# Optimization experiments

Measured on AMD Instinct MI355X. Metric: run time of the kernel, lower is better.

Reference implementation:

```python
import jax, jax.numpy as jnp
import numpy as np

D_MODEL = 2048
NUM_HEADS = 16
D_K = D_MODEL // NUM_HEADS
MAX_SEQ_LEN = 2048


def setup_inputs() -> dict:
    key = jax.random.key(0)
    ks = jax.random.split(key, 9)
    s = 1.0 / np.sqrt(D_MODEL)
    x = jax.random.normal(ks[0], (4, 2048, D_MODEL), dtype=jnp.float32)
    Wq = jax.random.normal(ks[1], (D_MODEL, D_MODEL), dtype=jnp.float32) * s
    bq = jnp.zeros((D_MODEL,), dtype=jnp.float32)
    Wk = jax.random.normal(ks[2], (D_MODEL, D_MODEL), dtype=jnp.float32) * s
    bk = jnp.zeros((D_MODEL,), dtype=jnp.float32)
    Wv = jax.random.normal(ks[3], (D_MODEL, D_MODEL), dtype=jnp.float32) * s
    bv = jnp.zeros((D_MODEL,), dtype=jnp.float32)
    Wo = jax.random.normal(ks[4], (D_MODEL, D_MODEL), dtype=jnp.float32) * s
    bo = jnp.zeros((D_MODEL,), dtype=jnp.float32)
    return {"x": x, "Wq": Wq, "bq": bq, "Wk": Wk, "bk": bk,
            "Wv": Wv, "bv": bv, "Wo": Wo, "bo": bo}


def _rope_tables(seq_len, d_k, dtype):
    # GPT-NeoX style rotate-half RoPE tables: [seq_len, d_k]
    inv_freq = 1.0 / (10000.0 ** (np.arange(0, d_k, 2, dtype=np.float32) / d_k))
    pos = np.arange(seq_len, dtype=np.float32)
    freqs = np.outer(pos, inv_freq)              # [S, d_k/2]
    emb = np.concatenate([freqs, freqs], axis=-1)  # [S, d_k]
    return jnp.asarray(np.cos(emb), dtype=dtype), jnp.asarray(np.sin(emb), dtype=dtype)


def _apply_rope(x, cos, sin):
    # x: [B, H, S, d_k]; rotate-half
    x1, x2 = jnp.split(x, 2, axis=-1)
    rotated = jnp.concatenate([-x2, x1], axis=-1)
    return x * cos + rotated * sin


def reference(x, Wq, bq, Wk, bk, Wv, bv, Wo, bo):
    B, S, _ = x.shape
    cos, sin = _rope_tables(S, D_K, x.dtype)  # [S, d_k]

    def split_heads(t):  # [B,S,D] -> [B,H,S,d_k]
        return t.reshape(B, S, NUM_HEADS, D_K).transpose(0, 2, 1, 3)

    q = split_heads(x @ Wq.T + bq)
    k = split_heads(x @ Wk.T + bk)
    v = split_heads(x @ Wv.T + bv)

    q = _apply_rope(q, cos, sin)
    k = _apply_rope(k, cos, sin)

    scale = 1.0 / jnp.sqrt(jnp.asarray(D_K, dtype=x.dtype))
    scores = jnp.einsum("bhqd,bhkd->bhqk", q, k) * scale
    attn = jax.nn.softmax(scores, axis=-1)
    out = jnp.einsum("bhqk,bhkd->bhqd", attn, v)  # [B,H,S,d_k]
    out = out.transpose(0, 2, 1, 3).reshape(B, S, D_MODEL)
    return out @ Wo.T + bo
```

## Files before the change

### kernel.cpp

```cpp
#include <hip/hip_runtime.h>
#include <hip/hip_bf16.h>
#include <math.h>

typedef __bf16 bf16;
typedef __bf16 bf16x2 __attribute__((ext_vector_type(2)));
typedef __bf16 bf16x4 __attribute__((ext_vector_type(4)));
typedef __bf16 bf16x8 __attribute__((ext_vector_type(8)));
typedef float f32x4 __attribute__((ext_vector_type(4)));

#define D_MODEL 2048
#define SEQ 2048
#define BATCH 4
#define NH 16
#define DK 128

typedef const __attribute__((address_space(1))) void* as1_ptr;
typedef __attribute__((address_space(3))) void* as3_ptr;

__device__ __forceinline__ void gld_lds16(const bf16* g, bf16* l) {
  __builtin_amdgcn_global_load_lds((as1_ptr)g, (as3_ptr)l, 16, 0, 0);
}

__global__ void cvt_kernel(const float* __restrict__ in, bf16* __restrict__ out, int n8) {
  int i = blockIdx.x * 256 + threadIdx.x;
  if (i >= n8) return;
  long base = (long)i * 8;
  const float4* p = (const float4*)(in + base);
  float4 a = p[0], b = p[1];
  bf16x8 v;
  v[0] = (bf16)a.x; v[1] = (bf16)a.y; v[2] = (bf16)a.z; v[3] = (bf16)a.w;
  v[4] = (bf16)b.x; v[5] = (bf16)b.y; v[6] = (bf16)b.z; v[7] = (bf16)b.w;
  *(bf16x8*)(out + base) = v;
}

__global__ void cvt4_kernel(const float* a, const float* b, const float* c, const float* d,
                            bf16* oa, bf16* ob, bf16* oc, bf16* od) {
  const float* in; bf16* out;
  switch (blockIdx.y) {
    case 0: in = a; out = oa; break;
    case 1: in = b; out = ob; break;
    case 2: in = c; out = oc; break;
    default: in = d; out = od; break;
  }
  int i = blockIdx.x * 256 + threadIdx.x;
  long base = (long)i * 8;
  const float4* p = (const float4*)(in + base);
  float4 x = p[0], y = p[1];
  bf16x8 v;
  v[0] = (bf16)x.x; v[1] = (bf16)x.y; v[2] = (bf16)x.z; v[3] = (bf16)x.w;
  v[4] = (bf16)y.x; v[5] = (bf16)y.y; v[6] = (bf16)y.z; v[7] = (bf16)y.w;
  *(bf16x8*)(out + base) = v;
}

template<int OUT_F32, int BIAS_ROW>
__global__ __launch_bounds__(256, 2)
void gemm_nt(const bf16* __restrict__ A, const bf16* __restrict__ B,
             const float* __restrict__ bias, void* __restrict__ Cout, int K, int ldc)
{
  __shared__ alignas(16) bf16 As[128 * 32];
  __shared__ alignas(16) bf16 Bs[128 * 32];
  const int tid  = threadIdx.x;
  const int wave = tid >> 6, lane = tid & 63;
  const int quad = lane >> 4, l16 = lane & 15;
  const int n0 = blockIdx.x * 128, m0 = blockIdx.y * 128;
  const int wm = (wave >> 1) * 64, wn = (wave & 1) * 64;

  const int srow = tid >> 2, scol = (tid & 3) * 8;
  const bf16* Ag1 = A + (long)(m0 + srow) * K + scol;
  const bf16* Ag2 = Ag1 + (long)64 * K;
  const bf16* Bg1 = B + (long)(n0 + srow) * K + scol;
  const bf16* Bg2 = Bg1 + (long)64 * K;
  bf16* Asw = As + wave * 512;
  bf16* Bsw = Bs + wave * 512;

  f32x4 acc[4][4] = {};
  for (int k0 = 0; k0 < K; k0 += 32) {
    __syncthreads();
    gld_lds16(Ag1 + k0, Asw);
    gld_lds16(Ag2 + k0, Asw + 2048);
    gld_lds16(Bg1 + k0, Bsw);
    gld_lds16(Bg2 + k0, Bsw + 2048);
    __syncthreads();
    bf16x8 Af[4], Bf[4];
    for (int mi = 0; mi < 4; mi++)
      Af[mi] = *(const bf16x8*)(&As[(wm + mi * 16 + l16) * 32 + quad * 8]);
    for (int ni = 0; ni < 4; ni++)
      Bf[ni] = *(const bf16x8*)(&Bs[(wn + ni * 16 + l16) * 32 + quad * 8]);
    for (int mi = 0; mi < 4; mi++)
      for (int ni = 0; ni < 4; ni++)
        acc[mi][ni] = __builtin_amdgcn_mfma_f32_16x16x32_bf16(Af[mi], Bf[ni], acc[mi][ni], 0, 0, 0);
  }

  float bv[4];
  if (!BIAS_ROW)
    for (int ni = 0; ni < 4; ni++) bv[ni] = bias[n0 + wn + ni * 16 + l16];
  for (int mi = 0; mi < 4; mi++)
    for (int r = 0; r < 4; r++) {
      long row = m0 + wm + mi * 16 + quad * 4 + r;
      float bm = BIAS_ROW ? bias[row] : 0.0f;
      for (int ni = 0; ni < 4; ni++) {
        float v = acc[mi][ni][r] + (BIAS_ROW ? bm : bv[ni]);
        long idx = row * (long)ldc + n0 + wn + ni * 16 + l16;
        if (OUT_F32) ((float*)Cout)[idx] = v;
        else         ((bf16*)Cout)[idx] = (bf16)v;
      }
    }
}

__global__ void ropetab_kernel(float* __restrict__ ctab) {
  int idx = blockIdx.x * 256 + threadIdx.x;
  int j = idx & 63, p = idx >> 6;
  float f = exp2f(-(float)j * 0.20762050593046f);
  float th = (float)p * f;
  ctab[idx * 2]     = cosf(th);
  ctab[idx * 2 + 1] = sinf(th);
}

__global__ void rope_kernel(bf16* __restrict__ Q, bf16* __restrict__ K,
                            const float* __restrict__ ctab) {
  long idx = (long)blockIdx.x * 256 + threadIdx.x;
  bf16* P = blockIdx.y ? K : Q;
  int i2 = (int)(idx & 31);
  int h  = (int)((idx >> 5) & 15);
  long row = idx >> 9;
  int pos = (int)(row & (SEQ - 1));
  float4 cs = *(const float4*)(ctab + ((long)pos * 64 + 2 * i2) * 2);
  long base = row * D_MODEL + h * DK + 2 * i2;
  bf16x2 x1 = *(bf16x2*)(P + base);
  bf16x2 x2 = *(bf16x2*)(P + base + 64);
  bf16x2 y1, y2;
  y1[0] = (bf16)((float)x1[0] * cs.x - (float)x2[0] * cs.y);
  y2[0] = (bf16)((float)x2[0] * cs.x + (float)x1[0] * cs.y);
  y1[1] = (bf16)((float)x1[1] * cs.z - (float)x2[1] * cs.w);
  y2[1] = (bf16)((float)x2[1] * cs.z + (float)x1[1] * cs.w);
  *(bf16x2*)(P + base)      = y1;
  *(bf16x2*)(P + base + 64) = y2;
}

__global__ __launch_bounds__(256, 2)
void attn_kernel(const bf16* __restrict__ Q, const bf16* __restrict__ K,
                 const bf16* __restrict__ Vt, bf16* __restrict__ O)
{
  __shared__ alignas(16) bf16 Ks[2][64 * 128];
  __shared__ alignas(16) bf16 Vts[2][128 * 64];
  __shared__ alignas(16) bf16 Ps[128 * 36];
  const int tid  = threadIdx.x;
  const int wave = tid >> 6, lane = tid & 63;
  const int quad = lane >> 4, l16 = lane & 15;
  const int qt = blockIdx.x, bh = blockIdx.y;
  const int b = bh >> 4, h = bh & 15;
  const long qrow0 = (long)b * SEQ + qt * 128;
  const bf16* Qb = Q + qrow0 * D_MODEL + h * DK;
  const bf16* Kb = K + (long)b * SEQ * D_MODEL + h * DK;
  const bf16* Vb = Vt + (long)(h * DK) * (BATCH * SEQ) + b * SEQ;

  bf16x8 Qf[2][4];
  for (int ni = 0; ni < 2; ni++)
    for (int ks = 0; ks < 4; ks++)
      Qf[ni][ks] = *(const bf16x8*)(Qb + (long)(wave * 32 + ni * 16 + l16) * D_MODEL + ks * 32 + quad * 8);

  const bf16* Ksrc[4]; const bf16* Vsrc[4];
  for (int i = 0; i < 4; i++) {
    int g = wave * 4 + i;
    int rk = 4 * g + (lane >> 4);
    int ck = l16 ^ (rk & 7);
    Ksrc[i] = Kb + (long)rk * D_MODEL + ck * 8;
    int rv = 8 * g + (lane >> 3);
    int cv = (lane & 7) ^ (rv & 7);
    Vsrc[i] = Vb + (long)rv * (BATCH * SEQ) + cv * 8;
  }

  f32x4 Oacc[8][2] = {};
  float lsum[2] = {0.0f, 0.0f};
  const float kSc = 0.088388347648318447f * 1.4426950408889634f;
  const int swz = l16 & 7;

  for (int i = 0; i < 4; i++) gld_lds16(Ksrc[i], &Ks[0][(wave * 4 + i) * 512]);
  for (int i = 0; i < 4; i++) gld_lds16(Vsrc[i], &Vts[0][(wave * 4 + i) * 512]);
  __syncthreads();

  int cur = 0;
  for (int kt = 64; kt <= SEQ; kt += 64) {
    if (kt < SEQ) {
      for (int i = 0; i < 4; i++)
        gld_lds16(Ksrc[i] + (long)kt * D_MODEL, &Ks[cur ^ 1][(wave * 4 + i) * 512]);
      for (int i = 0; i < 4; i++)
        gld_lds16(Vsrc[i] + kt, &Vts[cur ^ 1][(wave * 4 + i) * 512]);
    }
    const bf16* Ksb = Ks[cur];
    const bf16* Vsb = Vts[cur];

    for (int hh = 0; hh < 2; hh++) {
      f32x4 Sc[2][2] = {};
      __builtin_amdgcn_s_setprio(1);
      for (int ks = 0; ks < 4; ks++) {
        bf16x8 Kf[2];
        for (int j = 0; j < 2; j++) {
          int si = hh * 2 + j;
          int c = (ks * 4 + quad) ^ swz;
          Kf[j] = *(const bf16x8*)(&Ksb[(si * 16 + l16) * 128 + c * 8]);
        }
        for (int j = 0; j < 2; j++)
          for (int ni = 0; ni < 2; ni++)
            Sc[j][ni] = __builtin_amdgcn_mfma_f32_16x16x32_bf16(Kf[j], Qf[ni][ks], Sc[j][ni], 0, 0, 0);
      }
      __builtin_amdgcn_s_setprio(0);

      for (int j = 0; j < 2; j++)
        for (int ni = 0; ni < 2; ni++) {
          bf16x4 pk;
          for (int r = 0; r < 4; r++) {
            float p = exp2f(Sc[j][ni][r] * kSc);
            lsum[ni] += p;
            pk[r] = (bf16)p;
          }
          *(bf16x4*)(&Ps[(wave * 32 + ni * 16 + l16) * 36 + j * 16 + quad * 4]) = pk;
        }

      __builtin_amdgcn_s_setprio(1);
      bf16x8 Pf[2];
      for (int ni = 0; ni < 2; ni++)
        Pf[ni] = *(const bf16x8*)(&Ps[(wave * 32 + ni * 16 + l16) * 36 + quad * 8]);
      for (int mi = 0; mi < 8; mi++) {
        int c = (hh * 4 + quad) ^ swz;
        bf16x8 Vf = *(const bf16x8*)(&Vsb[(mi * 16 + l16) * 64 + c * 8]);
        for (int ni = 0; ni < 2; ni++)
          Oacc[mi][ni] = __builtin_amdgcn_mfma_f32_16x16x32_bf16(Vf, Pf[ni], Oacc[mi][ni], 0, 0, 0);
      }
      __builtin_amdgcn_s_setprio(0);
    }

    __syncthreads();
    cur ^= 1;
  }

  for (int ni = 0; ni < 2; ni++) {
    lsum[ni] += __shfl_xor(lsum[ni], 16);
    lsum[ni] += __shfl_xor(lsum[ni], 32);
  }

  for (int ni = 0; ni < 2; ni++) {
    float rinv = 1.0f / lsum[ni];
    long rowbase = (qrow0 + wave * 32 + ni * 16 + l16) * (long)D_MODEL + h * DK + quad * 4;
    for (int mi = 0; mi < 8; mi++) {
      bf16x4 o;
      for (int r = 0; r < 4; r++) o[r] = (bf16)(Oacc[mi][ni][r] * rinv);
      *(bf16x4*)(O + rowbase + mi * 16) = o;
    }
  }
}

extern "C" void kernel_launch(void* const* d_in, const int* in_sizes, int n_in,
                              void* d_out, int out_size, void* d_ws, size_t ws_size,
                              hipStream_t stream) {
  const float* x  = (const float*)d_in[0];
  const float* Wq = (const float*)d_in[1];
  const float* bq = (const float*)d_in[2];
  const float* Wk = (const float*)d_in[3];
  const float* bk = (const float*)d_in[4];
  const float* Wv = (const float*)d_in[5];
  const float* bv = (const float*)d_in[6];
  const float* Wo = (const float*)d_in[7];
  const float* bo = (const float*)d_in[8];
  float* out = (float*)d_out;

  bf16* ws = (bf16*)d_ws;
  bf16* xb  = ws;
  bf16* Wqb = ws + 16777216;
  bf16* Wkb = ws + 20971520;
  bf16* Wvb = ws + 25165824;
  bf16* Wob = ws + 29360128;
  bf16* Qp  = ws + 33554432;
  bf16* Kp  = ws + 50331648;
  bf16* VtF = ws + 67108864;
  float* ctab = (float*)ws;
  bf16* O   = xb;

  cvt_kernel<<<8192, 256, 0, stream>>>(x, xb, 2097152);
  cvt4_kernel<<<dim3(2048, 4), 256, 0, stream>>>(Wq, Wk, Wv, Wo, Wqb, Wkb, Wvb, Wob);

  dim3 gg(16, 64);
  gemm_nt<0, 0><<<gg, 256, 0, stream>>>(xb, Wqb, bq, Qp, 2048, 2048);
  gemm_nt<0, 0><<<gg, 256, 0, stream>>>(xb, Wkb, bk, Kp, 2048, 2048);
  gemm_nt<0, 1><<<dim3(64, 16), 256, 0, stream>>>(Wvb, xb, bv, VtF, 2048, 8192);

  ropetab_kernel<<<512, 256, 0, stream>>>(ctab);
  rope_kernel<<<dim3(16384, 2), 256, 0, stream>>>(Qp, Kp, ctab);

  attn_kernel<<<dim3(16, 64), 256, 0, stream>>>(Qp, Kp, VtF, O);

  gemm_nt<1, 0><<<gg, 256, 0, stream>>>(O, Wob, bo, out, 2048, 2048);
}
```

Baseline: 697.4 us.

## Replace GEMM with 256x256 tiled, double-buffered, swizzled LDS kernel

```diff
diff --git a/kernel.cpp b/kernel.cpp
--- a/kernel.cpp
+++ b/kernel.cpp
@@ -53,48 +53,93 @@
 }
 
 template<int OUT_F32, int BIAS_ROW>
-__global__ __launch_bounds__(256, 2)
-void gemm_nt(const bf16* __restrict__ A, const bf16* __restrict__ B,
+__global__ __launch_bounds__(512, 2)
+void gemm256(const bf16* __restrict__ A, const bf16* __restrict__ B,
              const float* __restrict__ bias, void* __restrict__ Cout, int K, int ldc)
 {
-  __shared__ alignas(16) bf16 As[128 * 32];
-  __shared__ alignas(16) bf16 Bs[128 * 32];
+  __shared__ alignas(16) bf16 As[2][256 * 64];
+  __shared__ alignas(16) bf16 Bs[2][256 * 64];
   const int tid  = threadIdx.x;
   const int wave = tid >> 6, lane = tid & 63;
   const int quad = lane >> 4, l16 = lane & 15;
-  const int n0 = blockIdx.x * 128, m0 = blockIdx.y * 128;
-  const int wm = (wave >> 1) * 64, wn = (wave & 1) * 64;
-
-  const int srow = tid >> 2, scol = (tid & 3) * 8;
-  const bf16* Ag1 = A + (long)(m0 + srow) * K + scol;
-  const bf16* Ag2 = Ag1 + (long)64 * K;
-  const bf16* Bg1 = B + (long)(n0 + srow) * K + scol;
-  const bf16* Bg2 = Bg1 + (long)64 * K;
-  bf16* Asw = As + wave * 512;
-  bf16* Bsw = Bs + wave * 512;
-
-  f32x4 acc[4][4] = {};
-  for (int k0 = 0; k0 < K; k0 += 32) {
-    __syncthreads();
-    gld_lds16(Ag1 + k0, Asw);
-    gld_lds16(Ag2 + k0, Asw + 2048);
-    gld_lds16(Bg1 + k0, Bsw);
-    gld_lds16(Bg2 + k0, Bsw + 2048);
-    __syncthreads();
-    bf16x8 Af[4], Bf[4];
-    for (int mi = 0; mi < 4; mi++)
-      Af[mi] = *(const bf16x8*)(&As[(wm + mi * 16 + l16) * 32 + quad * 8]);
-    for (int ni = 0; ni < 4; ni++)
-      Bf[ni] = *(const bf16x8*)(&Bs[(wn + ni * 16 + l16) * 32 + quad * 8]);
-    for (int mi = 0; mi < 4; mi++)
+  const int n0 = blockIdx.x * 256, m0 = blockIdx.y * 256;
+  const int wm = (wave >> 2) * 128, wn = (wave & 3) * 64;
+
+  const bf16* Asrc[4]; const bf16* Bsrc[4];
+  for (int i = 0; i < 4; i++) {
+    int g = wave * 4 + i;
+    int r = g * 8 + (lane >> 3);
+    int c = (lane & 7) ^ (r & 7);
+    Asrc[i] = A + (long)(m0 + r) * K + c * 8;
+    Bsrc[i] = B + (long)(n0 + r) * K + c * 8;
+  }
+
+  f32x4 acc[8][4] = {};
+  const int nt = K / 64;
+
+  for (int i = 0; i < 4; i++) gld_lds16(Asrc[i],      &As[0][(wave * 4 + i) * 512]);
+  for (int i = 0; i < 4; i++) gld_lds16(Bsrc[i],      &Bs[0][(wave * 4 + i) * 512]);
+  for (int i = 0; i < 4; i++) gld_lds16(Asrc[i] + 64, &As[1][(wave * 4 + i) * 512]);
+  for (int i = 0; i < 4; i++) gld_lds16(Bsrc[i] + 64, &Bs[1][(wave * 4 + i) * 512]);
+
+  for (int t = 0; t < nt; t++) {
+    const int cur = t & 1;
+    asm volatile("s_waitcnt vmcnt(8)" ::: "memory");
+    __builtin_amdgcn_s_barrier();
+    const bf16* Ab = As[cur];
+    const bf16* Bb = Bs[cur];
+
+    bf16x8 Af[8], Bf[4];
+    for (int mi = 0; mi < 8; mi++) {
+      int ra = wm + mi * 16 + l16;
+      int ch = quad ^ (ra & 7);
+      Af[mi] = *(const bf16x8*)(&Ab[ra * 64 + ch * 8]);
+    }
+    for (int ni = 0; ni < 4; ni++) {
+      int rb = wn + ni * 16 + l16;
+      int ch = quad ^ (rb & 7);
+      Bf[ni] = *(const bf16x8*)(&Bb[rb * 64 + ch * 8]);
+    }
+    asm volatile("s_waitcnt lgkmcnt(0)" ::: "memory");
+    __builtin_amdgcn_sched_barrier(0);
+    __builtin_amdgcn_s_setprio(1);
+    for (int mi = 0; mi < 8; mi++)
       for (int ni = 0; ni < 4; ni++)
         acc[mi][ni] = __builtin_amdgcn_mfma_f32_16x16x32_bf16(Af[mi], Bf[ni], acc[mi][ni], 0, 0, 0);
-  }
+    __builtin_amdgcn_s_setprio(0);
+
+    for (int mi = 0; mi < 8; mi++) {
+      int ra = wm + mi * 16 + l16;
+      int ch = (4 + quad) ^ (ra & 7);
+      Af[mi] = *(const bf16x8*)(&Ab[ra * 64 + ch * 8]);
+    }
+    for (int ni = 0; ni < 4; ni++) {
+      int rb = wn + ni * 16 + l16;
+      int ch = (4 + quad) ^ (rb & 7);
+      Bf[ni] = *(const bf16x8*)(&Bb[rb * 64 + ch * 8]);
+    }
+    asm volatile("s_waitcnt lgkmcnt(0)" ::: "memory");
+    __builtin_amdgcn_sched_barrier(0);
+    __builtin_amdgcn_s_barrier();
+
+    {
+      long k0 = (long)((t + 2 < nt) ? (t + 2) : (nt - 1)) * 64;
+      for (int i = 0; i < 4; i++) gld_lds16(Asrc[i] + k0, &As[cur][(wave * 4 + i) * 512]);
+      for (int i = 0; i < 4; i++) gld_lds16(Bsrc[i] + k0, &Bs[cur][(wave * 4 + i) * 512]);
+    }
+
+    __builtin_amdgcn_s_setprio(1);
+    for (int mi = 0; mi < 8; mi++)
+      for (int ni = 0; ni < 4; ni++)
+        acc[mi][ni] = __builtin_amdgcn_mfma_f32_16x16x32_bf16(Af[mi], Bf[ni], acc[mi][ni], 0, 0, 0);
+    __builtin_amdgcn_s_setprio(0);
+  }
+  asm volatile("s_waitcnt vmcnt(0)" ::: "memory");
 
   float bv[4];
   if (!BIAS_ROW)
     for (int ni = 0; ni < 4; ni++) bv[ni] = bias[n0 + wn + ni * 16 + l16];
-  for (int mi = 0; mi < 4; mi++)
+  for (int mi = 0; mi < 8; mi++)
     for (int r = 0; r < 4; r++) {
       long row = m0 + wm + mi * 16 + quad * 4 + r;
       float bm = BIAS_ROW ? bias[row] : 0.0f;
@@ -279,15 +324,14 @@
   cvt_kernel<<<8192, 256, 0, stream>>>(x, xb, 2097152);
   cvt4_kernel<<<dim3(2048, 4), 256, 0, stream>>>(Wq, Wk, Wv, Wo, Wqb, Wkb, Wvb, Wob);
 
-  dim3 gg(16, 64);
-  gemm_nt<0, 0><<<gg, 256, 0, stream>>>(xb, Wqb, bq, Qp, 2048, 2048);
-  gemm_nt<0, 0><<<gg, 256, 0, stream>>>(xb, Wkb, bk, Kp, 2048, 2048);
-  gemm_nt<0, 1><<<dim3(64, 16), 256, 0, stream>>>(Wvb, xb, bv, VtF, 2048, 8192);
+  gemm256<0, 0><<<dim3(8, 32), 512, 0, stream>>>(xb, Wqb, bq, Qp, 2048, 2048);
+  gemm256<0, 0><<<dim3(8, 32), 512, 0, stream>>>(xb, Wkb, bk, Kp, 2048, 2048);
+  gemm256<0, 1><<<dim3(32, 8), 512, 0, stream>>>(Wvb, xb, bv, VtF, 2048, 8192);
 
   ropetab_kernel<<<512, 256, 0, stream>>>(ctab);
   rope_kernel<<<dim3(16384, 2), 256, 0, stream>>>(Qp, Kp, ctab);
 
   attn_kernel<<<dim3(16, 64), 256, 0, stream>>>(Qp, Kp, VtF, O);
 
-  gemm_nt<1, 0><<<gg, 256, 0, stream>>>(O, Wob, bo, out, 2048, 2048);
-}
+  gemm256<1, 0><<<dim3(8, 32), 512, 0, stream>>>(O, Wob, bo, out, 2048, 2048);
+}
```

New measurement: 627.7 us. -10.0%, faster.
